# Kernel optimization log

Hardware: AMD Instinct MI355X
Metric: run time of the kernel (lower is better)

The kernel has to match this reference:

```python
import jax, jax.numpy as jnp
import numpy as np


def quat_to_rotmat(q):
    # q: [N,4] (w, x, y, z), normalized first (standard 3D-GS Transform)
    q = q / jnp.linalg.norm(q, axis=-1, keepdims=True)
    w, x, y, z = q[:, 0], q[:, 1], q[:, 2], q[:, 3]
    # rows of the 3x3 rotation matrix, stacked -> [N,3,3]
    r00 = 1 - 2 * (y * y + z * z)
    r01 = 2 * (x * y - w * z)
    r02 = 2 * (x * z + w * y)
    r10 = 2 * (x * y + w * z)
    r11 = 1 - 2 * (x * x + z * z)
    r12 = 2 * (y * z - w * x)
    r20 = 2 * (x * z - w * y)
    r21 = 2 * (y * z + w * x)
    r22 = 1 - 2 * (x * x + y * y)
    R = jnp.stack([
        jnp.stack([r00, r01, r02], axis=-1),
        jnp.stack([r10, r11, r12], axis=-1),
        jnp.stack([r20, r21, r22], axis=-1),
    ], axis=-2)
    return R


def setup_inputs() -> dict:
    key = jax.random.key(0)
    k1, k2 = jax.random.split(key)
    N = 4_000_000
    rotation = jax.random.normal(k1, (N, 4), dtype=jnp.float32)
    scale = jax.random.uniform(k2, (N, 3), dtype=jnp.float32)
    return {"rotation": rotation, "scale": scale}


def reference(rotation, scale):
    # get_covariance: M = R @ diag(scale); cov = M @ M^T  (symmetric PSD [N,3,3])
    R = quat_to_rotmat(rotation)          # [N,3,3]
    M = R * scale[:, None, :]             # R @ diag(scale), fused (no bmm)
    cov = jnp.einsum('nij,nkj->nik', M, M)  # M @ M^T
    return cov
```

## Files before the change

kernel.cpp:

```cpp
#include <hip/hip_runtime.h>


__global__ __launch_bounds__(256) void cov_main_kernel(
    const float4* __restrict__ rot4,
    const float4* __restrict__ scale4,
    float4* __restrict__ out4)
{
    __shared__ float s_scale[768];
    __shared__ __align__(16) float s_out[2304];
    const int t = threadIdx.x;
    const long long b = blockIdx.x;

    if (t < 192) {
        ((float4*)s_scale)[t] = scale4[b * 192 + t];
    }
    float4 q = rot4[b * 256 + t];
    __syncthreads();

    const float s0 = s_scale[t * 3 + 0];
    const float s1 = s_scale[t * 3 + 1];
    const float s2 = s_scale[t * 3 + 2];

    const float invn = rsqrtf(q.x * q.x + q.y * q.y + q.z * q.z + q.w * q.w);
    const float w = q.x * invn, x = q.y * invn, y = q.z * invn, z = q.w * invn;

    const float r00 = 1.f - 2.f * (y * y + z * z);
    const float r01 = 2.f * (x * y - w * z);
    const float r02 = 2.f * (x * z + w * y);
    const float r10 = 2.f * (x * y + w * z);
    const float r11 = 1.f - 2.f * (x * x + z * z);
    const float r12 = 2.f * (y * z - w * x);
    const float r20 = 2.f * (x * z - w * y);
    const float r21 = 2.f * (y * z + w * x);
    const float r22 = 1.f - 2.f * (x * x + y * y);

    const float m00 = r00 * s0, m01 = r01 * s1, m02 = r02 * s2;
    const float m10 = r10 * s0, m11 = r11 * s1, m12 = r12 * s2;
    const float m20 = r20 * s0, m21 = r21 * s1, m22 = r22 * s2;

    const float c00 = m00 * m00 + m01 * m01 + m02 * m02;
    const float c01 = m00 * m10 + m01 * m11 + m02 * m12;
    const float c02 = m00 * m20 + m01 * m21 + m02 * m22;
    const float c11 = m10 * m10 + m11 * m11 + m12 * m12;
    const float c12 = m10 * m20 + m11 * m21 + m12 * m22;
    const float c22 = m20 * m20 + m21 * m21 + m22 * m22;

    float* so = &s_out[t * 9];
    so[0] = c00; so[1] = c01; so[2] = c02;
    so[3] = c01; so[4] = c11; so[5] = c12;
    so[6] = c02; so[7] = c12; so[8] = c22;
    __syncthreads();

    const float4* sv = (const float4*)s_out;
    float4* ob = out4 + b * 576;
    ob[t]       = sv[t];
    ob[t + 256] = sv[t + 256];
    if (t < 64) ob[t + 512] = sv[t + 512];
}

__global__ void cov_tail_kernel(
    const float* __restrict__ rot,
    const float* __restrict__ scale,
    float* __restrict__ out,
    int start, int n)
{
    int i = start + blockIdx.x * blockDim.x + threadIdx.x;
    if (i >= n) return;
    const float qw = rot[i * 4 + 0], qx = rot[i * 4 + 1];
    const float qy = rot[i * 4 + 2], qz = rot[i * 4 + 3];
    const float s0 = scale[i * 3 + 0], s1 = scale[i * 3 + 1], s2 = scale[i * 3 + 2];
    const float invn = rsqrtf(qw * qw + qx * qx + qy * qy + qz * qz);
    const float w = qw * invn, x = qx * invn, y = qy * invn, z = qz * invn;
    const float r00 = 1.f - 2.f * (y * y + z * z);
    const float r01 = 2.f * (x * y - w * z);
    const float r02 = 2.f * (x * z + w * y);
    const float r10 = 2.f * (x * y + w * z);
    const float r11 = 1.f - 2.f * (x * x + z * z);
    const float r12 = 2.f * (y * z - w * x);
    const float r20 = 2.f * (x * z - w * y);
    const float r21 = 2.f * (y * z + w * x);
    const float r22 = 1.f - 2.f * (x * x + y * y);
    const float m00 = r00 * s0, m01 = r01 * s1, m02 = r02 * s2;
    const float m10 = r10 * s0, m11 = r11 * s1, m12 = r12 * s2;
    const float m20 = r20 * s0, m21 = r21 * s1, m22 = r22 * s2;
    float* o = out + (size_t)i * 9;
    o[0] = m00 * m00 + m01 * m01 + m02 * m02;
    o[1] = m00 * m10 + m01 * m11 + m02 * m12;
    o[2] = m00 * m20 + m01 * m21 + m02 * m22;
    o[3] = o[1];
    o[4] = m10 * m10 + m11 * m11 + m12 * m12;
    o[5] = m10 * m20 + m11 * m21 + m12 * m22;
    o[6] = o[2];
    o[7] = o[5];
    o[8] = m20 * m20 + m21 * m21 + m22 * m22;
}

extern "C" void kernel_launch(void* const* d_in, const int* in_sizes, int n_in,
                              void* d_out, int out_size, void* d_ws, size_t ws_size,
                              hipStream_t stream) {
    const float* rot   = (const float*)d_in[0];
    const float* scale = (const float*)d_in[1];
    float* out = (float*)d_out;

    const int N = in_sizes[0] / 4;
    const int nfull = N / 256;
    const int rem_start = nfull * 256;
    const int rem = N - rem_start;

    if (nfull > 0) {
        cov_main_kernel<<<nfull, 256, 0, stream>>>(
            (const float4*)rot, (const float4*)scale, (float4*)out);
    }
    if (rem > 0) {
        cov_tail_kernel<<<(rem + 255) / 256, 256, 0, stream>>>(
            rot, scale, out, rem_start, N);
    }
}
```

Baseline: 226.2 us.

## Use persistent grid-stride blocks with double-buffered shared output and prefetch

Replaces the one-tile-per-block launch with a fixed grid of 2048 persistent blocks that stride over tiles. Each block prefetches the next tile's quaternion and scale while it writes the current tile's output from a double-buffered shared array, which leaves one barrier per tile. Scale is now read with per-thread strided scalar loads instead of coalesced float4 staging through shared memory. This could make input loads less efficient, and a capped grid may lower the number of loads in flight on a purely bandwidth-bound kernel.

```diff
diff --git a/kernel.cpp b/kernel.cpp
--- a/kernel.cpp
+++ b/kernel.cpp
@@ -1,26 +1,10 @@
 #include <hip/hip_runtime.h>
 
 
-__global__ __launch_bounds__(256) void cov_main_kernel(
-    const float4* __restrict__ rot4,
-    const float4* __restrict__ scale4,
-    float4* __restrict__ out4)
+__device__ __forceinline__ void cov_from_quat(
+    const float4 q, const float s0, const float s1, const float s2,
+    float* __restrict__ so)
 {
-    __shared__ float s_scale[768];
-    __shared__ __align__(16) float s_out[2304];
-    const int t = threadIdx.x;
-    const long long b = blockIdx.x;
-
-    if (t < 192) {
-        ((float4*)s_scale)[t] = scale4[b * 192 + t];
-    }
-    float4 q = rot4[b * 256 + t];
-    __syncthreads();
-
-    const float s0 = s_scale[t * 3 + 0];
-    const float s1 = s_scale[t * 3 + 1];
-    const float s2 = s_scale[t * 3 + 2];
-
     const float invn = rsqrtf(q.x * q.x + q.y * q.y + q.z * q.z + q.w * q.w);
     const float w = q.x * invn, x = q.y * invn, y = q.z * invn, z = q.w * invn;
 
@@ -45,17 +29,52 @@
     const float c12 = m10 * m20 + m11 * m21 + m12 * m22;
     const float c22 = m20 * m20 + m21 * m21 + m22 * m22;
 
-    float* so = &s_out[t * 9];
     so[0] = c00; so[1] = c01; so[2] = c02;
     so[3] = c01; so[4] = c11; so[5] = c12;
     so[6] = c02; so[7] = c12; so[8] = c22;
-    __syncthreads();
+}
 
-    const float4* sv = (const float4*)s_out;
-    float4* ob = out4 + b * 576;
-    ob[t]       = sv[t];
-    ob[t + 256] = sv[t + 256];
-    if (t < 64) ob[t + 512] = sv[t + 512];
+__global__ __launch_bounds__(256) void cov_main_kernel(
+    const float4* __restrict__ rot4,
+    const float* __restrict__ scale,
+    float4* __restrict__ out4,
+    int ntiles)
+{
+    __shared__ __align__(16) float s_out[2][2304];
+    const int t = threadIdx.x;
+    const int stride = gridDim.x;
+
+    int tile = blockIdx.x;
+    if (tile >= ntiles) return;
+
+    float4 q = rot4[(long long)tile * 256 + t];
+    const float* sp = scale + ((long long)tile * 256 + t) * 3;
+    float s0 = sp[0], s1 = sp[1], s2 = sp[2];
+
+    int p = 0;
+    for (;;) {
+        cov_from_quat(q, s0, s1, s2, &s_out[p][t * 9]);
+
+        const int next = tile + stride;
+        const bool more = next < ntiles;
+        if (more) {
+            q = rot4[(long long)next * 256 + t];
+            const float* sp2 = scale + ((long long)next * 256 + t) * 3;
+            s0 = sp2[0]; s1 = sp2[1]; s2 = sp2[2];
+        }
+
+        __syncthreads();
+
+        const float4* sv = (const float4*)s_out[p];
+        float4* ob = out4 + (long long)tile * 576;
+        ob[t]       = sv[t];
+        ob[t + 256] = sv[t + 256];
+        if (t < 64) ob[t + 512] = sv[t + 512];
+
+        if (!more) break;
+        tile = next;
+        p ^= 1;
+    }
 }
 
 __global__ void cov_tail_kernel(
@@ -103,13 +122,14 @@
     float* out = (float*)d_out;
 
     const int N = in_sizes[0] / 4;
-    const int nfull = N / 256;
-    const int rem_start = nfull * 256;
+    const int ntiles = N / 256;
+    const int rem_start = ntiles * 256;
     const int rem = N - rem_start;
 
-    if (nfull > 0) {
-        cov_main_kernel<<<nfull, 256, 0, stream>>>(
-            (const float4*)rot, (const float4*)scale, (float4*)out);
+    if (ntiles > 0) {
+        const int grid = ntiles < 2048 ? ntiles : 2048;
+        cov_main_kernel<<<grid, 256, 0, stream>>>(
+            (const float4*)rot, scale, (float4*)out, ntiles);
     }
     if (rem > 0) {
         cov_tail_kernel<<<(rem + 255) / 256, 256, 0, stream>>>(
```

Measured after the change: 230.5 us. Within noise of the previous version (+1.9%).
